# Performance work log

Hardware: AMD Instinct MI355X
Metric: run time of the kernel (lower is better)

## Reference

```python
import jax, jax.numpy as jnp
import numpy as np

N = 16384
C_IN = 128
C_OUT = 128
S_DIM = 4
P_DIM = 32
K = 16


def setup_inputs() -> dict:
    key = jax.random.key(0)
    ks = jax.random.split(key, 8)
    lim = lambda fan_in: 1.0 / np.sqrt(fan_in)
    u = lambda k_, shape, b: jax.random.uniform(k_, shape, jnp.float32, -b, b)
    return {
        "x": jax.random.normal(ks[0], (N, C_IN), jnp.float32),
        "Ws": u(ks[1], (S_DIM, C_IN), lim(C_IN)),
        "bs": u(ks[2], (S_DIM,), lim(C_IN)),
        "Wh": u(ks[3], (P_DIM, C_IN), lim(C_IN)),
        "bh": u(ks[4], (P_DIM,), lim(C_IN)),
        "W1": u(ks[5], (C_OUT, C_IN), lim(C_IN)),
        "W2": u(ks[6], (C_OUT, 2 * P_DIM), lim(2 * P_DIM)),
        "b2": u(ks[7], (C_OUT,), lim(2 * P_DIM)),
        "k": K,
    }


def reference(x, Ws, bs, Wh, bh, W1, W2, b2, k):
    # latent space positions and message vectors
    s = x @ Ws.T + bs            # [N, S]
    h = x @ Wh.T + bh            # [N, P]
    # squared-distance matrix via Gram trick (monotone in true distance,
    # so k-NN indices match torch.cdist + topk(largest=False))
    sq = jnp.sum(s * s, axis=-1)                         # [N]
    d2 = sq[:, None] + sq[None, :] - 2.0 * (s @ s.T)     # [N, N]
    _, idx = jax.lax.top_k(-d2, k)                       # [N, k] neighbour ids (incl. self)
    # exact squared latent distance to selected neighbours (as in torch code)
    s_j = s[idx]                                          # [N, k, S]
    w = jnp.exp(-10.0 * jnp.sum((s[:, None, :] - s_j) ** 2, axis=-1))  # [N, k]
    msg = h[idx] * w[..., None]                           # [N, k, P]
    agg = jnp.concatenate([msg.mean(axis=1), msg.max(axis=1)], axis=-1)  # [N, 2P]
    return x @ W1.T + agg @ W2.T + b2                     # [N, C_OUT]
```

## Files before the change

### kernel.cpp

```cpp
#include <hip/hip_runtime.h>
#include <hip/hip_bf16.h>


#define NPTS 16384
#define CIN  128
#define SD   4
#define PD   32
#define KNN  16
#define COUT 128
#define FLTMAX 3.4028234663852886e+38f
#define NBIN 33
#define QPB  8
#define QCAP 512
#define MCAP 192
#define EPAD 1e-3f

typedef float v2f __attribute__((ext_vector_type(2)));
typedef unsigned int uint;
typedef unsigned long long u64;
typedef unsigned short u16;
typedef __attribute__((ext_vector_type(8))) short bf16x8;
typedef __attribute__((ext_vector_type(16))) float f32x16;

#define WS_S4     0
#define WS_H      0x40000
#define WS_AGG_M  0x280000
#define WS_SA     0x280000
#define WS_SB     0x300000
#define WS_WT_M   0x680000
#define WS_MASK   0x700000
#define WS_NEED_M 0x2700000
#define WS_CJ_F   0x400000
#define WS_AGG_F  0xC00000
#define WS_WT_F   0x1000000
#define JS   16
#define TJF  (NPTS/JS)

__device__ __forceinline__ float d2f(const float4 a, const float4 b) {
  v2f d0 = {a.x - b.x, a.y - b.y};
  v2f d1 = {a.z - b.z, a.w - b.w};
  v2f pr = d0*d0 + d1*d1;
  return pr.x + pr.y;
}

__device__ __forceinline__ u16 f2bf(float x) {
  uint u = __float_as_uint(x);
  uint r = (u + 0x7FFFu + ((u >> 16) & 1u)) >> 16;
  return (u16)r;
}
__device__ __forceinline__ float bf2f(u16 h) {
  return __uint_as_float(((uint)h) << 16);
}

__global__ __launch_bounds__(256) void k1_proj(
    const float* __restrict__ x, const float* __restrict__ Ws, const float* __restrict__ bs,
    const float* __restrict__ Wh, const float* __restrict__ bh,
    float4* __restrict__ s4, float* __restrict__ h) {
  __shared__ float  lw[36*128];
  __shared__ float  lx[64*132];
  __shared__ double rs[3*64*5];
  __shared__ float  rh[3*64*33];
  const int t = threadIdx.x;
  const int row0 = blockIdx.x * 64;
  for (int i2 = t; i2 < 36*128; i2 += 256)
    lw[i2] = (i2 < 512) ? Ws[i2] : Wh[i2 - 512];
#pragma unroll
  for (int g = 0; g < 8; ++g) {
    int fi = g*256 + t;
    int r = fi >> 5, c4 = fi & 31;
    *(float4*)&lx[r*132 + c4*4] = *(const float4*)&x[(size_t)(row0 + r)*CIN + c4*4];
  }
  __syncthreads();
  const int kq = t >> 6;
  const int r  = t & 63;
  const int kb = kq * 32;
  double sacc[4] = {0.0, 0.0, 0.0, 0.0};
  float  hacc[32];
#pragma unroll
  for (int p = 0; p < 32; ++p) hacc[p] = 0.f;
#pragma unroll
  for (int k4 = 0; k4 < 8; ++k4) {
    float4 xv = *(const float4*)&lx[r*132 + kb + k4*4];
    int kg = kb + k4*4;
#pragma unroll
    for (int p = 0; p < 4; ++p) {
      float4 wv = *(const float4*)&lw[p*128 + kg];
      sacc[p] = fma((double)xv.x, (double)wv.x, sacc[p]);
      sacc[p] = fma((double)xv.y, (double)wv.y, sacc[p]);
      sacc[p] = fma((double)xv.z, (double)wv.z, sacc[p]);
      sacc[p] = fma((double)xv.w, (double)wv.w, sacc[p]);
    }
#pragma unroll
    for (int p = 0; p < 32; ++p) {
      float4 wv = *(const float4*)&lw[(4+p)*128 + kg];
      hacc[p] = fmaf(xv.x, wv.x, fmaf(xv.y, wv.y, fmaf(xv.z, wv.z, fmaf(xv.w, wv.w, hacc[p]))));
    }
  }
  if (kq > 0) {
    const int bq = kq - 1;
#pragma unroll
    for (int d = 0; d < 4; ++d) rs[(bq*64 + r)*5 + d] = sacc[d];
#pragma unroll
    for (int p = 0; p < 32; ++p) rh[(bq*64 + r)*33 + p] = hacc[p];
  }
  __syncthreads();
  if (kq == 0) {
    const int row = row0 + r;
    float so[4];
#pragma unroll
    for (int d = 0; d < 4; ++d) {
      double sd = sacc[d] + rs[(0*64 + r)*5 + d] + rs[(1*64 + r)*5 + d]
                + rs[(2*64 + r)*5 + d] + (double)bs[d];
      so[d] = (float)sd;
    }
    s4[row] = make_float4(so[0], so[1], so[2], so[3]);
#pragma unroll
    for (int p4 = 0; p4 < 8; ++p4) {
      float o[4];
#pragma unroll
      for (int c = 0; c < 4; ++c) {
        int p = p4*4 + c;
        o[c] = hacc[p] + rh[(0*64 + r)*33 + p] + rh[(1*64 + r)*33 + p]
             + rh[(2*64 + r)*33 + p] + bh[p];
      }
      *(float4*)&h[(size_t)row*PD + p4*4] = make_float4(o[0], o[1], o[2], o[3]);
    }
  }
}

__global__ __launch_bounds__(256) void k2t_thresh(
    const float4* __restrict__ s4, uint4* __restrict__ sA, uint4* __restrict__ sB) {
  __shared__ float4 tile[2064];
  __shared__ uint   lhist[256*NBIN];
  const int t = threadIdx.x;
#pragma unroll
  for (int g = 0; g < 8; ++g) {
    int j = g*256 + t;
    tile[j + (j >> 7)] = s4[j];
  }
#pragma unroll
  for (int b = 0; b < NBIN; ++b) lhist[t*NBIN + b] = 0u;
  const int ql = t >> 4, tq = t & 15;
  const int q  = blockIdx.x*16 + ql;
  const float4 sq = s4[q];
  __syncthreads();
  float tau = d2f(sq, tile[tq*129]);
#pragma unroll
  for (int m = 1; m < 16; m <<= 1) tau = fmaxf(tau, __shfl_xor(tau, m, 16));
  const int ktop = (int)(__float_as_uint(tau) >> 21);
  const int hb = t*NBIN;
#pragma unroll 4
  for (int u = 0; u < 128; ++u) {
    float4 p = tile[tq*129 + u];
    float e = d2f(sq, p);
    int key = (int)(__float_as_uint(e) >> 21);
    int rel = ktop - key;
    rel = rel < 0 ? 0 : (rel > 32 ? 32 : rel);
    atomicAdd(&lhist[hb + rel], 1u);
  }
  __syncthreads();
  uint c0 = 0, c1 = 0;
  const int qb = ql*16;
  for (int u = 0; u < 16; ++u) {
    c0 += lhist[(qb + u)*NBIN + tq*2];
    c1 += (tq*2 + 1 < NBIN) ? lhist[(qb + u)*NBIN + tq*2 + 1] : 0u;
  }
  int S = (int)(c0 + c1);
#pragma unroll
  for (int d = 1; d < 16; d <<= 1) {
    int v = __shfl_down(S, d, 16);
    S += (tq + d < 16) ? v : 0;
  }
  int g = -1;
  if (S >= KNN) g = 2*tq;
  if (S - (int)c0 >= KNN) g = 2*tq + 1;
#pragma unroll
  for (int m = 1; m < 16; m <<= 1) g = max(g, __shfl_xor(g, m, 16));
  if (tq == 0) {
    uint K = (uint)(ktop - g);
    const float tv = __uint_as_float((K << 21) | 0x1FFFFFu);
    float sv[4] = {sq.x, sq.y, sq.z, sq.w};
    const float n2 = sq.x*sq.x + sq.y*sq.y + sq.z*sq.z + sq.w*sq.w;
    u16 hbv[4], lbv[4];
#pragma unroll
    for (int d = 0; d < 4; ++d) {
      u16 hh = f2bf(sv[d]);
      hbv[d] = hh;
      lbv[d] = f2bf(sv[d] - bf2f(hh));
    }
    const float aq = -0.5f*(n2 - tv) + EPAD;
    const float bn = -0.5f*n2;
    u16 aqh = f2bf(aq); u16 aql = f2bf(aq - bf2f(aqh));
    u16 bnh = f2bf(bn); u16 bnl = f2bf(bn - bf2f(bnh));
    const uint oneone = 0x3F803F80u;
    uint a0 = (uint)hbv[0] | ((uint)hbv[1] << 16);
    uint a1 = (uint)hbv[2] | ((uint)hbv[3] << 16);
    uint l0 = (uint)lbv[0] | ((uint)lbv[1] << 16);
    uint l1 = (uint)lbv[2] | ((uint)lbv[3] << 16);
    uint aqw = (uint)aqh | ((uint)aql << 16);
    uint bnw = (uint)bnh | ((uint)bnl << 16);
    uint4 A0; A0.x = a0; A0.y = a1; A0.z = a0; A0.w = a1;
    uint4 A1; A1.x = l0; A1.y = l1; A1.z = oneone; A1.w = aqw;
    uint4 B0; B0.x = a0; B0.y = a1; B0.z = l0; B0.w = l1;
    uint4 B1; B1.x = a0; B1.y = a1; B1.z = bnw; B1.w = oneone;
    sA[(size_t)q*2]     = A0;
    sA[(size_t)q*2 + 1] = A1;
    sB[(size_t)q*2]     = B0;
    sB[(size_t)q*2 + 1] = B1;
  }
}

__device__ __forceinline__ uint packbits16(const f32x16 a, const int shft) {
  uint b[4];
#pragma unroll
  for (int g = 0; g < 4; ++g) {
    uint bg = 0u;
#pragma unroll
    for (int e = 3; e >= 0; --e)
      bg = bg + bg + ((~__float_as_uint(a[4*g + e])) >> 31);
    b[g] = bg;
  }
  return (b[0] | (b[1] << 8) | (b[2] << 16) | (b[3] << 24)) << shft;
}

__global__ __launch_bounds__(256) void k2b_mfma(
    const u16* __restrict__ sA, const u16* __restrict__ sB, uint4* __restrict__ maskw) {
  __shared__ u16 lB[1024*16];
  const int t   = threadIdx.x;
  const int wv  = t >> 6, ln = t & 63;
  const int l31 = ln & 31, hi = ln >> 5;
  const int qbase = (blockIdx.x >> 4) * 256 + wv * 64;
  const int j0    = (blockIdx.x & 15) * 1024;
  for (int r = t; r < 1024; r += 256) {
    const uint4* src = (const uint4*)&sB[(size_t)(j0 + r)*16];
    uint4 v0 = src[0], v1 = src[1];
    *(uint4*)&lB[r*16]     = v0;
    *(uint4*)&lB[r*16 + 8] = v1;
  }
  const bf16x8 qf0 = *(const bf16x8*)&sA[(size_t)(qbase + l31)*16 + hi*8];
  const bf16x8 qf1 = *(const bf16x8*)&sA[(size_t)(qbase + 32 + l31)*16 + hi*8];
  __syncthreads();
  const int sh = hi * 4;
  const f32x16 zc = {0.f,0.f,0.f,0.f,0.f,0.f,0.f,0.f,0.f,0.f,0.f,0.f,0.f,0.f,0.f,0.f};
#pragma unroll 1
  for (int cc = 0; cc < 8; ++cc) {
    uint w0[4], w1[4];
#pragma unroll
    for (int jt = 0; jt < 4; ++jt) {
      const bf16x8 af = *(const bf16x8*)&lB[(cc*128 + jt*32 + l31)*16 + hi*8];
      f32x16 a0 = __builtin_amdgcn_mfma_f32_32x32x16_bf16(af, qf0, zc, 0, 0, 0);
      f32x16 a1 = __builtin_amdgcn_mfma_f32_32x32x16_bf16(af, qf1, zc, 0, 0, 0);
      w0[jt] = packbits16(a0, sh);
      w1[jt] = packbits16(a1, sh);
    }
    uint of[4];
#pragma unroll
    for (int jt = 0; jt < 4; ++jt) {
      uint f0 = w0[jt] | (uint)__shfl_xor((int)w0[jt], 32);
      uint f1 = w1[jt] | (uint)__shfl_xor((int)w1[jt], 32);
      of[jt] = hi ? f1 : f0;
    }
    const int c = (blockIdx.x & 15)*8 + cc;
    uint4 o; o.x = of[0]; o.y = of[1]; o.z = of[2]; o.w = of[3];
    maskw[(size_t)c*NPTS + qbase + ln] = o;
  }
}

__global__ __launch_bounds__(256) void k3_sel2(
    const float4* __restrict__ s4, const float* __restrict__ h,
    const uint4* __restrict__ maskw, float* __restrict__ agg) {
  __shared__ unsigned short jl[QPB*QCAP];
  __shared__ u16  cls[QPB*QCAP];
  __shared__ u64  qbuf[QPB*MCAP];
  __shared__ u64  win[QPB*KNN];
  __shared__ uint hist[QPB*32];
  __shared__ uint cnts[QPB];
  __shared__ uint mc[QPB];
  const int t  = threadIdx.x;
  const int ql = t >> 5, ln = t & 31;
  const int q  = blockIdx.x*QPB + ql;
  if (ln == 0) { cnts[ql] = 0u; mc[ql] = 0u; }
  hist[ql*32 + ln] = 0u;
  if (ln < KNN) win[ql*KNN + ln] = 0ull;
  const float4 sq = s4[q];
  __syncthreads();
  const int qa = t & 7;
  const int cg = t >> 3;
  uint4 m[4];
#pragma unroll
  for (int u = 0; u < 4; ++u)
    m[u] = maskw[(size_t)(cg + u*32)*NPTS + blockIdx.x*QPB + qa];
  int pc = 0;
#pragma unroll
  for (int u = 0; u < 4; ++u)
    pc += __popc(m[u].x) + __popc(m[u].y) + __popc(m[u].z) + __popc(m[u].w);
  int base = (int)atomicAdd(&cnts[qa], (uint)pc);
#pragma unroll
  for (int u = 0; u < 4; ++u) {
    uint wvs[4] = {m[u].x, m[u].y, m[u].z, m[u].w};
#pragma unroll
    for (int w = 0; w < 4; ++w) {
      uint bits = wvs[w];
      const int jb = (cg + u*32)*128 + w*32;
      while (bits) {
        int b = __builtin_ctz(bits); bits &= bits - 1;
        if (base < QCAP) jl[qa*QCAP + base] = (unsigned short)(jb + b);
        ++base;
      }
    }
  }
  __syncthreads();
  const int cnt = min((int)cnts[ql], QCAP);
  uint kmax = 0u;
  {
    int u = ln;
    for (; u + 32 < cnt; u += 64) {
      int ja = jl[ql*QCAP + u];
      int jb = jl[ql*QCAP + u + 32];
      float ea = d2f(sq, s4[ja]);
      float eb = d2f(sq, s4[jb]);
      uint ca = __float_as_uint(ea) >> 21;
      uint cb = __float_as_uint(eb) >> 21;
      cls[ql*QCAP + u]      = (u16)ca;
      cls[ql*QCAP + u + 32] = (u16)cb;
      kmax = max(kmax, max(ca, cb));
    }
    if (u < cnt) {
      int j = jl[ql*QCAP + u];
      float e = d2f(sq, s4[j]);
      uint cv = __float_as_uint(e) >> 21;
      cls[ql*QCAP + u] = (u16)cv;
      kmax = max(kmax, cv);
    }
  }
#pragma unroll
  for (int m2 = 1; m2 < 32; m2 <<= 1) kmax = max(kmax, (uint)__shfl_xor((int)kmax, m2, 32));
  for (int u = ln; u < cnt; u += 32) {
    uint cv = cls[ql*QCAP + u];
    uint rel = min(kmax - cv, 31u);
    atomicAdd(&hist[ql*32 + rel], 1u);
  }
  __syncthreads();
  uint cum = hist[ql*32 + ln];
#pragma unroll
  for (int d = 1; d < 32; d <<= 1) {
    uint v = (uint)__shfl_down((int)cum, d, 32);
    if (ln + d < 32) cum += v;
  }
  const uint need = (uint)(cnt < KNN ? cnt : KNN);
  u64 bal = __ballot(cum >= need);
  uint half = (uint)(bal >> (((t >> 5) & 1) * 32));
  const uint rstar = 31u - (uint)__builtin_clz(half);
  const uint bcls = kmax - rstar;
  __syncthreads();
  for (int u = ln; u < cnt; u += 32) {
    if ((uint)cls[ql*QCAP + u] <= bcls) {
      int j = jl[ql*QCAP + u];
      float e = d2f(sq, s4[j]);
      u64 key = ((u64)__float_as_uint(e) << 14) | (uint)j;
      uint pos = atomicAdd(&mc[ql], 1u);
      if (pos < MCAP) qbuf[ql*MCAP + pos] = key;
    }
  }
  __syncthreads();
  const int mcnt = (int)mc[ql];
  if (mcnt <= MCAP) {
    for (int w = ln; w < mcnt; w += 32) {
      u64 key = qbuf[ql*MCAP + w];
      int rank = 0;
      for (int v = 0; v < mcnt; ++v) rank += (qbuf[ql*MCAP + v] < key) ? 1 : 0;
      if (rank < KNN) win[ql*KNN + rank] = key;
    }
  } else {
    for (int u = ln; u < cnt; u += 32) {
      if ((uint)cls[ql*QCAP + u] <= bcls) {
        int j = jl[ql*QCAP + u];
        float e = d2f(sq, s4[j]);
        u64 key = ((u64)__float_as_uint(e) << 14) | (uint)j;
        int rank = 0;
        for (int v = 0; v < cnt; ++v) {
          int jv = jl[ql*QCAP + v];
          float ev = d2f(sq, s4[jv]);
          u64 kv2 = ((u64)__float_as_uint(ev) << 14) | (uint)jv;
          rank += (kv2 < key) ? 1 : 0;
        }
        if (rank < KNN) win[ql*KNN + rank] = key;
      }
    }
  }
  __syncthreads();
  float sum = 0.f, mx = -FLTMAX;
#pragma unroll
  for (int r4 = 0; r4 < 4; ++r4) {
    u64 k0 = win[ql*KNN + r4*4 + 0];
    u64 k1 = win[ql*KNN + r4*4 + 1];
    u64 k2 = win[ql*KNN + r4*4 + 2];
    u64 k3v = win[ql*KNN + r4*4 + 3];
    int j0 = (int)(k0 & 16383u), j1 = (int)(k1 & 16383u);
    int j2 = (int)(k2 & 16383u), j3 = (int)(k3v & 16383u);
    float h0 = h[(size_t)j0*PD + ln];
    float h1 = h[(size_t)j1*PD + ln];
    float h2 = h[(size_t)j2*PD + ln];
    float h3 = h[(size_t)j3*PD + ln];
    float w0 = __expf(-10.f * __uint_as_float((uint)(k0 >> 14)));
    float w1 = __expf(-10.f * __uint_as_float((uint)(k1 >> 14)));
    float w2 = __expf(-10.f * __uint_as_float((uint)(k2 >> 14)));
    float w3 = __expf(-10.f * __uint_as_float((uint)(k3v >> 14)));
    float m0 = w0*h0, m1 = w1*h1, m2 = w2*h2, m3 = w3*h3;
    sum += m0 + m1 + m2 + m3;
    mx = fmaxf(mx, fmaxf(fmaxf(m0, m1), fmaxf(m2, m3)));
  }
  agg[(size_t)q*64 + ln]      = sum * 0.0625f;
  agg[(size_t)q*64 + 32 + ln] = mx;
}

__global__ __launch_bounds__(256) void k2_knn_fb(
    const float4* __restrict__ s4, unsigned short* __restrict__ cand_j) {
  __shared__ float4 tile[TJF];
  __shared__ int    lbuf[256*33];
  const int t  = threadIdx.x;
  const int ib = blockIdx.x & 31;
  const int jc = blockIdx.x >> 5;
  const int jbase = jc * TJF;
#pragma unroll
  for (int g = 0; g < 4; ++g) tile[g*256 + t] = s4[jbase + g*256 + t];
  const int ia = ib*256 + t;
  const int ic = ia + 8192;
  const float4 sa = s4[ia];
  const float4 sc = s4[ic];
  __syncthreads();
  float va[KNN], vb[KNN]; int ja[KNN], jb[KNN];
#pragma unroll
  for (int q = 0; q < KNN; ++q) { va[q] = FLTMAX; ja[q] = 0; vb[q] = FLTMAX; jb[q] = 0; }
  float cma = FLTMAX, cmb = FLTMAX;
  int cpa = 0, cpb = 0, ca = 0, cb = 0;
  auto insertA = [&](float e, int jj) {
#pragma unroll
    for (int q = 0; q < KNN; ++q) if (q == cpa) { va[q] = e; ja[q] = jj; }
    cma = va[0]; cpa = 0;
#pragma unroll
    for (int q = 1; q < KNN; ++q) { if (va[q] > cma) { cma = va[q]; cpa = q; } }
  };
  auto insertB = [&](float e, int jj) {
#pragma unroll
    for (int q = 0; q < KNN; ++q) if (q == cpb) { vb[q] = e; jb[q] = jj; }
    cmb = vb[0]; cpb = 0;
#pragma unroll
    for (int q = 1; q < KNN; ++q) { if (vb[q] > cmb) { cmb = vb[q]; cpb = q; } }
  };
  auto compactA = [&]() {
    for (int u = 0; u < ca; ++u) {
      int jj = lbuf[t*33 + u];
      float e = d2f(sa, tile[jj]);
      if (e < cma) insertA(e, jj);
    }
    ca = 0;
  };
  auto compactB = [&]() {
    for (int u = 0; u < cb; ++u) {
      int jj = lbuf[t*33 + 16 + u];
      float e = d2f(sc, tile[jj]);
      if (e < cmb) insertB(e, jj);
    }
    cb = 0;
  };
  for (int ob = 0; ob < TJF/8; ++ob) {
#pragma unroll
    for (int u = 0; u < 8; ++u) {
      int jj = ob*8 + u;
      float4 p = tile[jj];
      float ea = d2f(sa, p);
      float eb = d2f(sc, p);
      if (ea < cma) { lbuf[t*33 + ca] = jj; ++ca; }
      if (eb < cmb) { lbuf[t*33 + 16 + cb] = jj; ++cb; }
    }
    if (__any(ca > 8)) compactA();
    if (__any(cb > 8)) compactB();
  }
  compactA(); compactB();
#pragma unroll
  for (int q = 0; q < KNN; ++q) {
    int c = jc*KNN + q;
    cand_j[(size_t)c*NPTS + ia] = (unsigned short)(ja[q] + jbase);
    cand_j[(size_t)c*NPTS + ic] = (unsigned short)(jb[q] + jbase);
  }
}

__global__ __launch_bounds__(256) void k3_merge_fb(
    const float4* __restrict__ s4, const float4* __restrict__ h4,
    const unsigned short* __restrict__ cand_j, float* __restrict__ agg) {
  __shared__ float le[64*67];
  __shared__ int   lj[64*67];
  const int t  = threadIdx.x;
  const int il = t & 63, tq = t >> 6;
  const int i  = blockIdx.x*64 + il;
  const float4 si = s4[i];
  float val[KNN]; int vid[KNN];
#pragma unroll
  for (int q = 0; q < KNN; ++q) { val[q] = FLTMAX; vid[q] = 0; }
  float cmax = FLTMAX; int cpos = 0;
  for (int u = 0; u < 64; ++u) {
    int c = tq*64 + u;
    int j = cand_j[(size_t)c*NPTS + i];
    float e = d2f(si, s4[j]);
    if (e < cmax) {
#pragma unroll
      for (int q = 0; q < KNN; ++q) if (q == cpos) { val[q] = e; vid[q] = j; }
      cmax = val[0]; cpos = 0;
#pragma unroll
      for (int q = 1; q < KNN; ++q) { if (val[q] > cmax) { cmax = val[q]; cpos = q; } }
    }
  }
#pragma unroll
  for (int q = 0; q < KNN; ++q) {
    le[il*67 + tq*16 + q] = val[q];
    lj[il*67 + tq*16 + q] = vid[q];
  }
  __syncthreads();
  if (t < 64) {
    float mv[KNN]; int mj[KNN];
#pragma unroll
    for (int q = 0; q < KNN; ++q) { mv[q] = FLTMAX; mj[q] = 0; }
    float cm2 = FLTMAX; int cp2 = 0;
    for (int u = 0; u < 64; ++u) {
      float e = le[t*67 + u];
      int   j = lj[t*67 + u];
      if (e < cm2) {
#pragma unroll
        for (int q = 0; q < KNN; ++q) if (q == cp2) { mv[q] = e; mj[q] = j; }
        cm2 = mv[0]; cp2 = 0;
#pragma unroll
        for (int q = 1; q < KNN; ++q) { if (mv[q] > cm2) { cm2 = mv[q]; cp2 = q; } }
      }
    }
#pragma unroll
    for (int q = 0; q < KNN; ++q) {
      le[t*67 + q] = __expf(-10.f * mv[q]);
      lj[t*67 + q] = mj[q];
    }
  }
  __syncthreads();
  float ms[8], mm[8];
#pragma unroll
  for (int p = 0; p < 8; ++p) { ms[p] = 0.f; mm[p] = -FLTMAX; }
#pragma unroll 1
  for (int q = 0; q < KNN; ++q) {
    float w = le[il*67 + q];
    int   j = lj[il*67 + q];
    float4 a = h4[(size_t)j*8 + tq*2];
    float4 b = h4[(size_t)j*8 + tq*2 + 1];
    float m0 = a.x*w, m1 = a.y*w, m2 = a.z*w, m3 = a.w*w;
    float m4 = b.x*w, m5 = b.y*w, m6 = b.z*w, m7 = b.w*w;
    ms[0] += m0; mm[0] = fmaxf(mm[0], m0);
    ms[1] += m1; mm[1] = fmaxf(mm[1], m1);
    ms[2] += m2; mm[2] = fmaxf(mm[2], m2);
    ms[3] += m3; mm[3] = fmaxf(mm[3], m3);
    ms[4] += m4; mm[4] = fmaxf(mm[4], m4);
    ms[5] += m5; mm[5] = fmaxf(mm[5], m5);
    ms[6] += m6; mm[6] = fmaxf(mm[6], m6);
    ms[7] += m7; mm[7] = fmaxf(mm[7], m7);
  }
  float4 o0 = make_float4(ms[0]*0.0625f, ms[1]*0.0625f, ms[2]*0.0625f, ms[3]*0.0625f);
  float4 o1 = make_float4(ms[4]*0.0625f, ms[5]*0.0625f, ms[6]*0.0625f, ms[7]*0.0625f);
  *(float4*)&agg[(size_t)i*64 + tq*8]      = o0;
  *(float4*)&agg[(size_t)i*64 + tq*8 + 4]  = o1;
  *(float4*)&agg[(size_t)i*64 + 32 + tq*8]     = make_float4(mm[0], mm[1], mm[2], mm[3]);
  *(float4*)&agg[(size_t)i*64 + 32 + tq*8 + 4] = make_float4(mm[4], mm[5], mm[6], mm[7]);
}

__global__ __launch_bounds__(256) void k4a_wt(
    const float* __restrict__ W1, const float* __restrict__ W2, float* __restrict__ wT) {
  int idx = blockIdx.x*256 + threadIdx.x;
  if (idx >= 192*COUT) return;
  int k = idx >> 7, c = idx & 127;
  float v = (k < 128) ? W1[(size_t)c*128 + k] : W2[(size_t)c*64 + (k - 128)];
  wT[(size_t)k*COUT + c] = v;
}

__global__ __launch_bounds__(256) void k4_out2(
    const float* __restrict__ x, const float* __restrict__ agg,
    const float* __restrict__ wT, const float* __restrict__ b2,
    float* __restrict__ out) {
  __shared__ float xa[32*192];
  const int t = threadIdx.x;
  const int row0 = blockIdx.x * 32;
#pragma unroll
  for (int g = 0; g < 4; ++g) {
    int fi = g*256 + t;
    int r = fi >> 5, c4 = fi & 31;
    *(float4*)&xa[r*192 + c4*4] = *(const float4*)&x[(size_t)(row0+r)*CIN + c4*4];
  }
#pragma unroll
  for (int g = 0; g < 2; ++g) {
    int fi = g*256 + t;
    int r = fi >> 4, c4 = fi & 15;
    *(float4*)&xa[r*192 + 128 + c4*4] = *(const float4*)&agg[(size_t)(row0+r)*64 + c4*4];
  }
  __syncthreads();
  const int c4 = t & 31;
  const int rg = t >> 5;
  float acc[4][4];
#pragma unroll
  for (int r = 0; r < 4; ++r) { acc[r][0]=0.f; acc[r][1]=0.f; acc[r][2]=0.f; acc[r][3]=0.f; }
  for (int k = 0; k < 192; k += 4) {
    float4 w0 = *(const float4*)&wT[(size_t)(k+0)*COUT + c4*4];
    float4 w1 = *(const float4*)&wT[(size_t)(k+1)*COUT + c4*4];
    float4 w2 = *(const float4*)&wT[(size_t)(k+2)*COUT + c4*4];
    float4 w3 = *(const float4*)&wT[(size_t)(k+3)*COUT + c4*4];
#pragma unroll
    for (int r = 0; r < 4; ++r) {
      float4 xv = *(const float4*)&xa[(rg*4 + r)*192 + k];
      acc[r][0] = fmaf(xv.x, w0.x, fmaf(xv.y, w1.x, fmaf(xv.z, w2.x, fmaf(xv.w, w3.x, acc[r][0]))));
      acc[r][1] = fmaf(xv.x, w0.y, fmaf(xv.y, w1.y, fmaf(xv.z, w2.y, fmaf(xv.w, w3.y, acc[r][1]))));
      acc[r][2] = fmaf(xv.x, w0.z, fmaf(xv.y, w1.z, fmaf(xv.z, w2.z, fmaf(xv.w, w3.z, acc[r][2]))));
      acc[r][3] = fmaf(xv.x, w0.w, fmaf(xv.y, w1.w, fmaf(xv.z, w2.w, fmaf(xv.w, w3.w, acc[r][3]))));
    }
  }
  float4 bias = *(const float4*)&b2[c4*4];
#pragma unroll
  for (int r = 0; r < 4; ++r) {
    float4 o = make_float4(acc[r][0]+bias.x, acc[r][1]+bias.y, acc[r][2]+bias.z, acc[r][3]+bias.w);
    *(float4*)&out[(size_t)(row0 + rg*4 + r)*COUT + c4*4] = o;
  }
}

extern "C" void kernel_launch(void* const* d_in, const int* in_sizes, int n_in,
                              void* d_out, int out_size, void* d_ws, size_t ws_size,
                              hipStream_t stream) {
  const float* x  = (const float*)d_in[0];
  const float* Ws = (const float*)d_in[1];
  const float* bs = (const float*)d_in[2];
  const float* Wh = (const float*)d_in[3];
  const float* bh = (const float*)d_in[4];
  const float* W1 = (const float*)d_in[5];
  const float* W2 = (const float*)d_in[6];
  const float* b2 = (const float*)d_in[7];
  float* out = (float*)d_out;

  char* ws = (char*)d_ws;
  float4* s4 = (float4*)(ws + WS_S4);
  float*  h  = (float*) (ws + WS_H);

  k1_proj<<<NPTS/64, 256, 0, stream>>>(x, Ws, bs, Wh, bh, s4, h);

  if (ws_size >= (size_t)WS_NEED_M) {
    float* agg = (float*)(ws + WS_AGG_M);
    float* wT  = (float*)(ws + WS_WT_M);
    uint4* sa  = (uint4*)(ws + WS_SA);
    uint4* sb  = (uint4*)(ws + WS_SB);
    uint4* mw  = (uint4*)(ws + WS_MASK);
    k2t_thresh<<<NPTS/16, 256, 0, stream>>>(s4, sa, sb);
    k2b_mfma<<<1024, 256, 0, stream>>>((const u16*)sa, (const u16*)sb, mw);
    k3_sel2<<<NPTS/QPB, 256, 0, stream>>>(s4, h, (const uint4*)mw, agg);
    k4a_wt<<<(192*COUT + 255)/256, 256, 0, stream>>>(W1, W2, wT);
    k4_out2<<<NPTS/32, 256, 0, stream>>>(x, agg, wT, b2, out);
  } else {
    unsigned short* cj = (unsigned short*)(ws + WS_CJ_F);
    float* agg = (float*)(ws + WS_AGG_F);
    float* wT  = (float*)(ws + WS_WT_F);
    k2_knn_fb<<<512, 256, 0, stream>>>(s4, cj);
    k3_merge_fb<<<NPTS/64, 256, 0, stream>>>(s4, (const float4*)h, cj, agg);
    k4a_wt<<<(192*COUT + 255)/256, 256, 0, stream>>>(W1, W2, wT);
    k4_out2<<<NPTS/32, 256, 0, stream>>>(x, agg, wT, b2, out);
  }
}
```

Before: 188.4 us.

## Fold weight transpose into threshold kernel, swizzle MFMA LDS, unroll distance loop

The W1/W2 transpose that fills wT is moved into the first 96 blocks of k2t_thresh, which removes a separate kernel launch. In k2b_mfma, the two 8-element halves of each LDS row are swapped depending on the row index, to spread the MFMA operand reads across LDS banks. In k3_sel2, the candidate distance loop now handles four candidates per iteration to expose more memory-level parallelism. These three changes are unrelated to each other; the fused transpose adds a small amount of work to the threshold kernel.

```diff
diff --git a/kernel.cpp b/kernel.cpp
--- a/kernel.cpp
+++ b/kernel.cpp
@@ -129,10 +129,17 @@
 }
 
 __global__ __launch_bounds__(256) void k2t_thresh(
-    const float4* __restrict__ s4, uint4* __restrict__ sA, uint4* __restrict__ sB) {
+    const float4* __restrict__ s4, uint4* __restrict__ sA, uint4* __restrict__ sB,
+    const float* __restrict__ W1, const float* __restrict__ W2, float* __restrict__ wT) {
   __shared__ float4 tile[2064];
   __shared__ uint   lhist[256*NBIN];
   const int t = threadIdx.x;
+  if (blockIdx.x < 96) {
+    int idx = blockIdx.x*256 + t;
+    int kk = idx >> 7, c = idx & 127;
+    float v = (kk < 128) ? W1[(size_t)c*128 + kk] : W2[(size_t)c*64 + (kk - 128)];
+    wT[(size_t)kk*COUT + c] = v;
+  }
 #pragma unroll
   for (int g = 0; g < 8; ++g) {
     int j = g*256 + t;
@@ -234,8 +241,9 @@
   for (int r = t; r < 1024; r += 256) {
     const uint4* src = (const uint4*)&sB[(size_t)(j0 + r)*16];
     uint4 v0 = src[0], v1 = src[1];
-    *(uint4*)&lB[r*16]     = v0;
-    *(uint4*)&lB[r*16 + 8] = v1;
+    const int sw = (r >> 2) & 1;
+    *(uint4*)&lB[r*16 + sw*8]       = v0;
+    *(uint4*)&lB[r*16 + (sw^1)*8]   = v1;
   }
   const bf16x8 qf0 = *(const bf16x8*)&sA[(size_t)(qbase + l31)*16 + hi*8];
   const bf16x8 qf1 = *(const bf16x8*)&sA[(size_t)(qbase + 32 + l31)*16 + hi*8];
@@ -247,7 +255,8 @@
     uint w0[4], w1[4];
 #pragma unroll
     for (int jt = 0; jt < 4; ++jt) {
-      const bf16x8 af = *(const bf16x8*)&lB[(cc*128 + jt*32 + l31)*16 + hi*8];
+      const int row = cc*128 + jt*32 + l31;
+      const bf16x8 af = *(const bf16x8*)&lB[row*16 + (hi ^ ((row >> 2) & 1))*8];
       f32x16 a0 = __builtin_amdgcn_mfma_f32_32x32x16_bf16(af, qf0, zc, 0, 0, 0);
       f32x16 a1 = __builtin_amdgcn_mfma_f32_32x32x16_bf16(af, qf1, zc, 0, 0, 0);
       w0[jt] = packbits16(a0, sh);
@@ -314,6 +323,25 @@
   uint kmax = 0u;
   {
     int u = ln;
+    for (; u + 96 < cnt; u += 128) {
+      int j0v = jl[ql*QCAP + u];
+      int j1v = jl[ql*QCAP + u + 32];
+      int j2v = jl[ql*QCAP + u + 64];
+      int j3v = jl[ql*QCAP + u + 96];
+      float e0 = d2f(sq, s4[j0v]);
+      float e1 = d2f(sq, s4[j1v]);
+      float e2 = d2f(sq, s4[j2v]);
+      float e3 = d2f(sq, s4[j3v]);
+      uint c0v = __float_as_uint(e0) >> 21;
+      uint c1v = __float_as_uint(e1) >> 21;
+      uint c2v = __float_as_uint(e2) >> 21;
+      uint c3v = __float_as_uint(e3) >> 21;
+      cls[ql*QCAP + u]      = (u16)c0v;
+      cls[ql*QCAP + u + 32] = (u16)c1v;
+      cls[ql*QCAP + u + 64] = (u16)c2v;
+      cls[ql*QCAP + u + 96] = (u16)c3v;
+      kmax = max(kmax, max(max(c0v, c1v), max(c2v, c3v)));
+    }
     for (; u + 32 < cnt; u += 64) {
       int ja = jl[ql*QCAP + u];
       int jb = jl[ql*QCAP + u + 32];
@@ -649,10 +677,9 @@
     uint4* sa  = (uint4*)(ws + WS_SA);
     uint4* sb  = (uint4*)(ws + WS_SB);
     uint4* mw  = (uint4*)(ws + WS_MASK);
-    k2t_thresh<<<NPTS/16, 256, 0, stream>>>(s4, sa, sb);
+    k2t_thresh<<<NPTS/16, 256, 0, stream>>>(s4, sa, sb, W1, W2, wT);
     k2b_mfma<<<1024, 256, 0, stream>>>((const u16*)sa, (const u16*)sb, mw);
     k3_sel2<<<NPTS/QPB, 256, 0, stream>>>(s4, h, (const uint4*)mw, agg);
-    k4a_wt<<<(192*COUT + 255)/256, 256, 0, stream>>>(W1, W2, wT);
     k4_out2<<<NPTS/32, 256, 0, stream>>>(x, agg, wT, b2, out);
   } else {
     unsigned short* cj = (unsigned short*)(ws + WS_CJ_F);
```

New measurement: 187.5 us. About the same (-0.5%).
